# Optimization experiments

Measured on AMD Instinct MI355X. Metric: run time of the kernel, lower is better.

Reference implementation:

```python
import jax, jax.numpy as jnp
import numpy as np

N1, N2, N3, N4, D = 50000, 100000, 200000, 300000, 256


def setup_inputs() -> dict:
    key = jax.random.key(0)
    ks = jax.random.split(key, 10)
    feat = jax.random.normal(ks[0], (N1, D), dtype=jnp.float32) * 0.5  # scaled so level-4 products stay bounded
    c2a = jax.random.randint(ks[1], (N2,), 0, N1)
    c2b = jax.random.randint(ks[2], (N2,), 0, N1)
    c3a = jax.random.randint(ks[3], (N3,), 0, N2)
    c3b = jax.random.randint(ks[4], (N3,), 0, N2)
    c4a = jax.random.randint(ks[5], (N4,), 0, N3)
    c4b = jax.random.randint(ks[6], (N4,), 0, N3)
    W = jax.random.normal(ks[7], (D, D), dtype=jnp.float32) / jnp.sqrt(jnp.float32(D))
    b = jax.random.normal(ks[8], (D,), dtype=jnp.float32) * 0.01
    return {"feat": feat, "c2a": c2a, "c2b": c2b, "c3a": c3a, "c3b": c3b,
            "c4a": c4a, "c4b": c4b, "W": W, "b": b}


def _scatter_sum(h_parent, ca, cb, num_children):
    # each parent sends its feature to both children; children sum incoming messages
    z = jnp.zeros((num_children, h_parent.shape[1]), dtype=h_parent.dtype)
    return z.at[ca].add(h_parent).at[cb].add(h_parent)


def reference(feat, c2a, c2b, c3a, c3b, c4a, c4b, W, b):
    # upward: prod reduction over the two constituent subpaths (mailbox prod, dim=1)
    h1 = feat
    h2 = h1[c2a] * h1[c2b]            # [N2, D]
    h3 = h2[c3a] * h2[c3b]            # [N3, D]
    h4 = h3[c4a] * h3[c4b]            # [N4, D]
    # downward: sum-scatter parent -> children, h = h + h_down
    h3 = h3 + _scatter_sum(h4, c4a, c4b, h3.shape[0])
    h2 = h2 + _scatter_sum(h3, c3a, c3b, h2.shape[0])
    h1 = h1 + _scatter_sum(h2, c2a, c2b, h1.shape[0])
    # apply_nodes on n1: Linear + SiLU
    out = jax.nn.silu(h1 @ W + b)
    return out
```

## Files before the change

### kernel.cpp

```cpp
#include <hip/hip_runtime.h>
#include <cstdint>
#include <cstddef>

#define DD 256
#define DH 128
#define SCAN_BLK 256
#define SCAN_ELEMS 2048

__device__ __forceinline__ float4 f4mul(float4 a, float4 b) {
    return make_float4(a.x * b.x, a.y * b.y, a.z * b.z, a.w * b.w);
}
__device__ __forceinline__ float4 f4add(float4 a, float4 b) {
    return make_float4(a.x + b.x, a.y + b.y, a.z + b.z, a.w + b.w);
}
__device__ __forceinline__ float4 ldh4(const float* __restrict__ base, int row, int sl) {
    return ((const float4*)(base + (size_t)row * DH))[sl];
}
__device__ __forceinline__ float4 ldf4(const float* __restrict__ base, int row, int doff, int sl) {
    return ((const float4*)(base + (size_t)row * DD + doff))[sl];
}

__global__ void k_count_all(const int* __restrict__ c2a, const int* __restrict__ c2b,
                            const int* __restrict__ c3a, const int* __restrict__ c3b,
                            const int* __restrict__ c4a, const int* __restrict__ c4b,
                            int n2, int n3, int n4,
                            int* __restrict__ cnt4, int* __restrict__ cnt3,
                            int* __restrict__ cnt2) {
    int e = blockIdx.x * blockDim.x + threadIdx.x;
    if (e < n4) { atomicAdd(&cnt4[c4a[e]], 1); atomicAdd(&cnt4[c4b[e]], 1); }
    if (e < n3) { atomicAdd(&cnt3[c3a[e]], 1); atomicAdd(&cnt3[c3b[e]], 1); }
    if (e < n2) { atomicAdd(&cnt2[c2a[e]], 1); atomicAdd(&cnt2[c2b[e]], 1); }
}

__global__ void k_fill_all(const int* __restrict__ c2a, const int* __restrict__ c2b,
                           const int* __restrict__ c3a, const int* __restrict__ c3b,
                           const int* __restrict__ c4a, const int* __restrict__ c4b,
                           int n2, int n3, int n4,
                           int* __restrict__ cur4, int* __restrict__ cur3,
                           int* __restrict__ cur2,
                           int2* __restrict__ entp, int* __restrict__ ent3,
                           int* __restrict__ ent2) {
    int e = blockIdx.x * blockDim.x + threadIdx.x;
    if (e < n4) {
        int a = c4a[e], b = c4b[e];
        int2 prA = make_int2(c3a[b], c3b[b]);
        int2 prB = make_int2(c3a[a], c3b[a]);
        int pa = atomicAdd(&cur4[a], 1);
        int pb = atomicAdd(&cur4[b], 1);
        entp[pa] = prA;
        entp[pb] = prB;
    }
    if (e < n3) {
        int a = c3a[e], b = c3b[e];
        int pa = atomicAdd(&cur3[a], 1);
        int pb = atomicAdd(&cur3[b], 1);
        ent3[pa] = e;
        ent3[pb] = e;
    }
    if (e < n2) {
        int a = c2a[e], b = c2b[e];
        int pa = atomicAdd(&cur2[a], 1);
        int pb = atomicAdd(&cur2[b], 1);
        ent2[pa] = e;
        ent2[pb] = e;
    }
}

__global__ void k_block_sums(const int* __restrict__ cnt, int n, int* __restrict__ bsum) {
    __shared__ int sdata[SCAN_BLK];
    int base = blockIdx.x * SCAN_ELEMS;
    int s = 0;
#pragma unroll
    for (int k = 0; k < 8; ++k) {
        int idx = base + threadIdx.x + k * SCAN_BLK;
        if (idx < n) s += cnt[idx];
    }
    sdata[threadIdx.x] = s;
    __syncthreads();
    for (int off = SCAN_BLK / 2; off > 0; off >>= 1) {
        if (threadIdx.x < off) sdata[threadIdx.x] += sdata[threadIdx.x + off];
        __syncthreads();
    }
    if (threadIdx.x == 0) bsum[blockIdx.x] = sdata[0];
}

__global__ void k_scan_bsums(int* __restrict__ bsum, int nb, int* __restrict__ total_out) {
    if (threadIdx.x == 0 && blockIdx.x == 0) {
        int acc = 0;
        for (int b = 0; b < nb; ++b) { int v = bsum[b]; bsum[b] = acc; acc += v; }
        *total_out = acc;
    }
}

__global__ void k_scan_final(const int* __restrict__ cnt, int n,
                             const int* __restrict__ bsum, int* __restrict__ offs,
                             int* __restrict__ cursor) {
    __shared__ int sdata[SCAN_BLK];
    int base = blockIdx.x * SCAN_ELEMS;
    int t0 = base + threadIdx.x * 8;
    int loc[8];
    int s = 0;
#pragma unroll
    for (int k = 0; k < 8; ++k) {
        int idx = t0 + k;
        int v = (idx < n) ? cnt[idx] : 0;
        loc[k] = s;
        s += v;
    }
    sdata[threadIdx.x] = s;
    __syncthreads();
    int run = s;
    for (int off = 1; off < SCAN_BLK; off <<= 1) {
        int add = (threadIdx.x >= (unsigned)off) ? sdata[threadIdx.x - off] : 0;
        __syncthreads();
        run += add;
        sdata[threadIdx.x] = run;
        __syncthreads();
    }
    int texcl = run - s + bsum[blockIdx.x];
#pragma unroll
    for (int k = 0; k < 8; ++k) {
        int idx = t0 + k;
        if (idx < n) {
            int v = texcl + loc[k];
            offs[idx] = v;
            cursor[idx] = v;
        }
    }
}

__global__ void k_h2_half(const float* __restrict__ feat, const int* __restrict__ c2a,
                          const int* __restrict__ c2b, float* __restrict__ h2h,
                          int n2, int doff) {
    int q = blockIdx.x * 8 + (threadIdx.x >> 5);
    int sl = threadIdx.x & 31;
    if (q >= n2) return;
    float4 v = f4mul(ldf4(feat, c2a[q], doff, sl), ldf4(feat, c2b[q], doff, sl));
    ((float4*)(h2h + (size_t)q * DH))[sl] = v;
}

__global__ void k_h3tot_half(const float* __restrict__ h2h,
                             const int* __restrict__ c3a, const int* __restrict__ c3b,
                             const int* __restrict__ offs4, const int2* __restrict__ entp,
                             float* __restrict__ h3th, int lo, int hi) {
    int j = lo + blockIdx.x * 8 + (threadIdx.x >> 5);
    int sl = threadIdx.x & 31;
    if (j >= hi) return;
    float4 own = f4mul(ldh4(h2h, c3a[j], sl), ldh4(h2h, c3b[j], sl));
    float4 s = make_float4(0.f, 0.f, 0.f, 0.f);
    int e0 = offs4[j], e1 = offs4[j + 1];
    int e = e0;
    for (; e + 1 < e1; e += 2) {
        int2 p0 = entp[e], p1 = entp[e + 1];
        float4 a0 = ldh4(h2h, p0.x, sl), b0 = ldh4(h2h, p0.y, sl);
        float4 a1 = ldh4(h2h, p1.x, sl), b1 = ldh4(h2h, p1.y, sl);
        s = f4add(s, f4add(f4mul(a0, b0), f4mul(a1, b1)));
    }
    if (e < e1) {
        int2 p = entp[e];
        s = f4add(s, f4mul(ldh4(h2h, p.x, sl), ldh4(h2h, p.y, sl)));
    }
    float4 r = f4mul(own, make_float4(1.f + s.x, 1.f + s.y, 1.f + s.z, 1.f + s.w));
    ((float4*)(h3th + (size_t)(j - lo) * DH))[sl] = r;
}

__global__ void k_m2_half(const float* __restrict__ h2h,
                          const int* __restrict__ offs3, const int* __restrict__ ent3,
                          const float* __restrict__ h3th, float* __restrict__ dst,
                          int n2, int lo, int hi, int first) {
    int q = blockIdx.x * 8 + (threadIdx.x >> 5);
    int sl = threadIdx.x & 31;
    if (q >= n2) return;
    float4 h = first ? ldh4(h2h, q, sl) : ldh4(dst, q, sl);
    int f0 = offs3[q], f1 = offs3[q + 1];
    int f = f0;
    for (; f + 1 < f1; f += 2) {
        int j0 = ent3[f], j1 = ent3[f + 1];
        bool in0 = (j0 >= lo) && (j0 < hi);
        bool in1 = (j1 >= lo) && (j1 < hi);
        if (in0 && in1) {
            h = f4add(h, f4add(ldh4(h3th, j0 - lo, sl), ldh4(h3th, j1 - lo, sl)));
        } else if (in0) {
            h = f4add(h, ldh4(h3th, j0 - lo, sl));
        } else if (in1) {
            h = f4add(h, ldh4(h3th, j1 - lo, sl));
        }
    }
    if (f < f1) {
        int j0 = ent3[f];
        if (j0 >= lo && j0 < hi) h = f4add(h, ldh4(h3th, j0 - lo, sl));
    }
    ((float4*)(dst + (size_t)q * DH))[sl] = h;
}

__global__ void k_h1_half(const float* __restrict__ feat, const float* __restrict__ m2,
                          const int* __restrict__ offs2, const int* __restrict__ ent2,
                          float* __restrict__ out, int n1, int doff) {
    int i = blockIdx.x * 8 + (threadIdx.x >> 5);
    int sl = threadIdx.x & 31;
    if (i >= n1) return;
    float4 h = ldf4(feat, i, doff, sl);
    int e0 = offs2[i], e1 = offs2[i + 1];
    int e = e0;
    for (; e + 1 < e1; e += 2) {
        int q0 = ent2[e], q1 = ent2[e + 1];
        h = f4add(h, f4add(ldh4(m2, q0, sl), ldh4(m2, q1, sl)));
    }
    if (e < e1) h = f4add(h, ldh4(m2, ent2[e], sl));
    ((float4*)(out + (size_t)i * DD + doff))[sl] = h;
}

__device__ __forceinline__ float silu_f(float x) { return x / (1.0f + expf(-x)); }

__global__ __launch_bounds__(256) void k_gemm_silu(float* __restrict__ h,
                                                   const float* __restrict__ W,
                                                   const float* __restrict__ bias,
                                                   int n1) {
    __shared__ float As[32 * DD];
    const int t = threadIdx.x;
    const int row0 = blockIdx.x * 32;

    const float4* hv = (const float4*)h;
    float4* As4 = (float4*)As;
#pragma unroll
    for (int i = 0; i < 8; ++i) {
        int idx = t + i * 256;
        int r = idx >> 6, c = idx & 63;
        int gr = row0 + r;
        float4 v = make_float4(0.f, 0.f, 0.f, 0.f);
        if (gr < n1) v = hv[(size_t)gr * 64 + c];
        As4[idx] = v;
    }
    __syncthreads();

    const int rg = t >> 6;
    const int cg = t & 63;
    const float4* Wv = (const float4*)W;

    float4 acc[8];
#pragma unroll
    for (int r = 0; r < 8; ++r) acc[r] = make_float4(0.f, 0.f, 0.f, 0.f);

    for (int k = 0; k < DD; k += 4) {
        float4 a[8];
#pragma unroll
        for (int r = 0; r < 8; ++r)
            a[r] = *(const float4*)&As[(rg * 8 + r) * DD + k];
#pragma unroll
        for (int kk = 0; kk < 4; ++kk) {
            float4 w = Wv[(size_t)(k + kk) * 64 + cg];
#pragma unroll
            for (int r = 0; r < 8; ++r) {
                float av = (kk == 0) ? a[r].x : (kk == 1) ? a[r].y
                         : (kk == 2) ? a[r].z : a[r].w;
                acc[r].x += av * w.x;
                acc[r].y += av * w.y;
                acc[r].z += av * w.z;
                acc[r].w += av * w.w;
            }
        }
    }

    float4 bb = ((const float4*)bias)[cg];
    float4* ho = (float4*)h;
#pragma unroll
    for (int r = 0; r < 8; ++r) {
        int gr = row0 + rg * 8 + r;
        if (gr >= n1) continue;
        float4 x = acc[r];
        x.x = silu_f(x.x + bb.x);
        x.y = silu_f(x.y + bb.y);
        x.z = silu_f(x.z + bb.z);
        x.w = silu_f(x.w + bb.w);
        ho[(size_t)gr * 64 + cg] = x;
    }
}

static inline size_t al16(size_t x) { return (x + 15) & ~(size_t)15; }

extern "C" void kernel_launch(void* const* d_in, const int* in_sizes, int n_in,
                              void* d_out, int out_size, void* d_ws, size_t ws_size,
                              hipStream_t stream) {
    const float* feat = (const float*)d_in[0];
    const int* c2a = (const int*)d_in[1];
    const int* c2b = (const int*)d_in[2];
    const int* c3a = (const int*)d_in[3];
    const int* c3b = (const int*)d_in[4];
    const int* c4a = (const int*)d_in[5];
    const int* c4b = (const int*)d_in[6];
    const float* W = (const float*)d_in[7];
    const float* bias = (const float*)d_in[8];

    const int N1 = in_sizes[0] / DD;
    const int N2 = in_sizes[1];
    const int N3 = in_sizes[3];
    const int N4 = in_sizes[5];
    float* out = (float*)d_out;
    char* ws = (char*)d_ws;

    dim3 blk(256);
    auto rows_grid8 = [](int n) { return dim3((unsigned)((n + 7) / 8)); };
    auto thr_grid = [](int n) { return dim3((unsigned)((n + 255) / 256)); };

    size_t cnt4_b  = al16((size_t)N3 * 4);
    size_t cnt3_b  = al16((size_t)N2 * 4);
    size_t cnt2_b  = al16((size_t)N1 * 4);
    size_t cur4_b  = al16((size_t)N3 * 4);
    size_t cur3_b  = al16((size_t)N2 * 4);
    size_t cur2_b  = al16((size_t)N1 * 4);
    size_t bsum_b  = al16(4096);
    size_t offs4_b = al16((size_t)(N3 + 1) * 4);
    size_t entp_b  = al16((size_t)2 * N4 * 8);
    size_t offs3_b = al16((size_t)(N2 + 1) * 4);
    size_t ent3_b  = al16((size_t)2 * N3 * 4);
    size_t offs2_b = al16((size_t)(N1 + 1) * 4);
    size_t ent2_b  = al16((size_t)2 * N2 * 4);
    size_t fixed_b = cnt4_b + cnt3_b + cnt2_b + cur4_b + cur3_b + cur2_b + bsum_b +
                     offs4_b + entp_b + offs3_b + ent3_b + offs2_b + ent2_b;
    size_t h2h_b = (size_t)N2 * DH * sizeof(float);
    size_t h3th_full_b = (size_t)N3 * DH * sizeof(float);

    char* p = ws;
    int* cnt4  = (int*)p; p += cnt4_b;
    int* cnt3  = (int*)p; p += cnt3_b;
    int* cnt2  = (int*)p; p += cnt2_b;
    int* cur4  = (int*)p; p += cur4_b;
    int* cur3  = (int*)p; p += cur3_b;
    int* cur2  = (int*)p; p += cur2_b;
    int* bsum  = (int*)p; p += bsum_b;
    int* offs4 = (int*)p; p += offs4_b;
    int2* entp = (int2*)p; p += entp_b;
    int* offs3 = (int*)p; p += offs3_b;
    int* ent3  = (int*)p; p += ent3_b;
    int* offs2 = (int*)p; p += offs2_b;
    int* ent2  = (int*)p; p += ent2_b;
    float* h2h = (float*)p; p += h2h_b;

    bool single = (ws_size >= fixed_b + h2h_b + h3th_full_b);

    auto scan_offs = [&](int* cn, int nnode, int* offs, int* cursor) {
        int nb = (nnode + SCAN_ELEMS - 1) / SCAN_ELEMS;
        k_block_sums<<<dim3((unsigned)nb), dim3(SCAN_BLK), 0, stream>>>(cn, nnode, bsum);
        k_scan_bsums<<<dim3(1), dim3(64), 0, stream>>>(bsum, nb, offs + nnode);
        k_scan_final<<<dim3((unsigned)nb), dim3(SCAN_BLK), 0, stream>>>(cn, nnode, bsum,
                                                                        offs, cursor);
    };

    int maxE = N2 > N3 ? N2 : N3;
    if (N4 > maxE) maxE = N4;
    hipMemsetAsync(cnt4, 0, cnt4_b + cnt3_b + cnt2_b, stream);
    k_count_all<<<thr_grid(maxE), blk, 0, stream>>>(c2a, c2b, c3a, c3b, c4a, c4b,
                                                    N2, N3, N4, cnt4, cnt3, cnt2);
    scan_offs(cnt4, N3, offs4, cur4);
    scan_offs(cnt3, N2, offs3, cur3);
    scan_offs(cnt2, N1, offs2, cur2);
    k_fill_all<<<thr_grid(maxE), blk, 0, stream>>>(c2a, c2b, c3a, c3b, c4a, c4b,
                                                   N2, N3, N4, cur4, cur3, cur2,
                                                   entp, ent3, ent2);

    if (single) {
        float* h3th = (float*)p;
        for (int doff = 0; doff < DD; doff += DH) {
            k_h2_half<<<rows_grid8(N2), blk, 0, stream>>>(feat, c2a, c2b, h2h, N2, doff);
            k_h3tot_half<<<rows_grid8(N3), blk, 0, stream>>>(h2h, c3a, c3b, offs4, entp,
                                                             h3th, 0, N3);
            k_m2_half<<<rows_grid8(N2), blk, 0, stream>>>(h2h, offs3, ent3, h3th,
                                                          h2h, N2, 0, N3, 1);
            k_h1_half<<<rows_grid8(N1), blk, 0, stream>>>(feat, h2h, offs2, ent2,
                                                          out, N1, doff);
        }
    } else {
        float* m2h = (float*)p;
        char* pc = p + h2h_b;
        float* h3th = (float*)pc;
        size_t free_b = (ws_size > fixed_b + 2 * h2h_b) ? ws_size - fixed_b - 2 * h2h_b : 0;
        int chunk_rows = (int)(free_b / ((size_t)DH * sizeof(float)));
        if (chunk_rows > N3) chunk_rows = N3;
        if (chunk_rows < 1) chunk_rows = 1;
        int C = (N3 + chunk_rows - 1) / chunk_rows;
        chunk_rows = (N3 + C - 1) / C;

        for (int doff = 0; doff < DD; doff += DH) {
            k_h2_half<<<rows_grid8(N2), blk, 0, stream>>>(feat, c2a, c2b, h2h, N2, doff);
            int first = 1;
            for (int lo = 0; lo < N3; lo += chunk_rows) {
                int hi = lo + chunk_rows;
                if (hi > N3) hi = N3;
                k_h3tot_half<<<rows_grid8(hi - lo), blk, 0, stream>>>(h2h, c3a, c3b,
                                                                      offs4, entp,
                                                                      h3th, lo, hi);
                k_m2_half<<<rows_grid8(N2), blk, 0, stream>>>(h2h, offs3, ent3, h3th,
                                                              m2h, N2, lo, hi, first);
                first = 0;
            }
            k_h1_half<<<rows_grid8(N1), blk, 0, stream>>>(feat, m2h, offs2, ent2,
                                                          out, N1, doff);
        }
    }

    k_gemm_silu<<<dim3((unsigned)((N1 + 31) / 32)), blk, 0, stream>>>(out, W, bias, N1);
}
```

Baseline: 777.6 us.

## Scatter parent values into CSR slot order so children read contiguous rows

The producer kernels now write each h3 and m2 row straight into the child's CSR slot positions (pos3/pos2, recorded during fill). The downward-sum kernels then stream contiguous rows instead of gathering through index lists. Vector width also drops from float4 over 32 lanes to float2 over 64 lanes, so one wavefront covers one row. The cost is a duplicated slot buffer (2x rows) and more workspace, and tiered fallbacks are kept for when the workspace is too small.

```diff
diff --git a/kernel.cpp b/kernel.cpp
--- a/kernel.cpp
+++ b/kernel.cpp
@@ -7,17 +7,17 @@
 #define SCAN_BLK 256
 #define SCAN_ELEMS 2048
 
-__device__ __forceinline__ float4 f4mul(float4 a, float4 b) {
-    return make_float4(a.x * b.x, a.y * b.y, a.z * b.z, a.w * b.w);
-}
-__device__ __forceinline__ float4 f4add(float4 a, float4 b) {
-    return make_float4(a.x + b.x, a.y + b.y, a.z + b.z, a.w + b.w);
-}
-__device__ __forceinline__ float4 ldh4(const float* __restrict__ base, int row, int sl) {
-    return ((const float4*)(base + (size_t)row * DH))[sl];
-}
-__device__ __forceinline__ float4 ldf4(const float* __restrict__ base, int row, int doff, int sl) {
-    return ((const float4*)(base + (size_t)row * DD + doff))[sl];
+__device__ __forceinline__ float2 mul2(float2 a, float2 b) {
+    return make_float2(a.x * b.x, a.y * b.y);
+}
+__device__ __forceinline__ float2 add2(float2 a, float2 b) {
+    return make_float2(a.x + b.x, a.y + b.y);
+}
+__device__ __forceinline__ float2 ldh(const float* __restrict__ base, int row, int lane) {
+    return ((const float2*)(base + (size_t)row * DH))[lane];
+}
+__device__ __forceinline__ float2 ldf(const float* __restrict__ base, int row, int doff, int lane) {
+    return ((const float2*)(base + (size_t)row * DD + doff))[lane];
 }
 
 __global__ void k_count_all(const int* __restrict__ c2a, const int* __restrict__ c2b,
@@ -39,7 +39,8 @@
                            int* __restrict__ cur4, int* __restrict__ cur3,
                            int* __restrict__ cur2,
                            int2* __restrict__ entp, int* __restrict__ ent3,
-                           int* __restrict__ ent2) {
+                           int* __restrict__ ent2,
+                           int* __restrict__ pos3, int* __restrict__ pos2) {
     int e = blockIdx.x * blockDim.x + threadIdx.x;
     if (e < n4) {
         int a = c4a[e], b = c4b[e];
@@ -56,6 +57,8 @@
         int pb = atomicAdd(&cur3[b], 1);
         ent3[pa] = e;
         ent3[pb] = e;
+        pos3[2 * e] = pa;
+        pos3[2 * e + 1] = pb;
     }
     if (e < n2) {
         int a = c2a[e], b = c2b[e];
@@ -63,6 +66,8 @@
         int pb = atomicAdd(&cur2[b], 1);
         ent2[pa] = e;
         ent2[pb] = e;
+        pos2[2 * e] = pa;
+        pos2[2 * e + 1] = pb;
     }
 }
 
@@ -132,46 +137,110 @@
 __global__ void k_h2_half(const float* __restrict__ feat, const int* __restrict__ c2a,
                           const int* __restrict__ c2b, float* __restrict__ h2h,
                           int n2, int doff) {
-    int q = blockIdx.x * 8 + (threadIdx.x >> 5);
-    int sl = threadIdx.x & 31;
+    int q = blockIdx.x * 4 + (threadIdx.x >> 6);
+    int lane = threadIdx.x & 63;
     if (q >= n2) return;
-    float4 v = f4mul(ldf4(feat, c2a[q], doff, sl), ldf4(feat, c2b[q], doff, sl));
-    ((float4*)(h2h + (size_t)q * DH))[sl] = v;
+    float2 v = mul2(ldf(feat, c2a[q], doff, lane), ldf(feat, c2b[q], doff, lane));
+    ((float2*)(h2h + (size_t)q * DH))[lane] = v;
+}
+
+__global__ void k_h3tot_slot(const float* __restrict__ h2h,
+                             const int* __restrict__ c3a, const int* __restrict__ c3b,
+                             const int* __restrict__ offs4, const int2* __restrict__ entp,
+                             const int* __restrict__ pos3, float* __restrict__ S3,
+                             int n3) {
+    int j = blockIdx.x * 4 + (threadIdx.x >> 6);
+    int lane = threadIdx.x & 63;
+    if (j >= n3) return;
+    float2 own = mul2(ldh(h2h, c3a[j], lane), ldh(h2h, c3b[j], lane));
+    float2 s = make_float2(0.f, 0.f);
+    int e0 = offs4[j], e1 = offs4[j + 1];
+    int e = e0;
+    for (; e + 1 < e1; e += 2) {
+        int2 p0 = entp[e], p1 = entp[e + 1];
+        float2 a0 = ldh(h2h, p0.x, lane), b0 = ldh(h2h, p0.y, lane);
+        float2 a1 = ldh(h2h, p1.x, lane), b1 = ldh(h2h, p1.y, lane);
+        s = add2(s, add2(mul2(a0, b0), mul2(a1, b1)));
+    }
+    if (e < e1) {
+        int2 p = entp[e];
+        s = add2(s, mul2(ldh(h2h, p.x, lane), ldh(h2h, p.y, lane)));
+    }
+    float2 r = mul2(own, make_float2(1.f + s.x, 1.f + s.y));
+    int s0 = pos3[2 * j], s1 = pos3[2 * j + 1];
+    ((float2*)(S3 + (size_t)s0 * DH))[lane] = r;
+    ((float2*)(S3 + (size_t)s1 * DH))[lane] = r;
 }
 
 __global__ void k_h3tot_half(const float* __restrict__ h2h,
                              const int* __restrict__ c3a, const int* __restrict__ c3b,
                              const int* __restrict__ offs4, const int2* __restrict__ entp,
                              float* __restrict__ h3th, int lo, int hi) {
-    int j = lo + blockIdx.x * 8 + (threadIdx.x >> 5);
-    int sl = threadIdx.x & 31;
+    int j = lo + blockIdx.x * 4 + (threadIdx.x >> 6);
+    int lane = threadIdx.x & 63;
     if (j >= hi) return;
-    float4 own = f4mul(ldh4(h2h, c3a[j], sl), ldh4(h2h, c3b[j], sl));
-    float4 s = make_float4(0.f, 0.f, 0.f, 0.f);
+    float2 own = mul2(ldh(h2h, c3a[j], lane), ldh(h2h, c3b[j], lane));
+    float2 s = make_float2(0.f, 0.f);
     int e0 = offs4[j], e1 = offs4[j + 1];
     int e = e0;
     for (; e + 1 < e1; e += 2) {
         int2 p0 = entp[e], p1 = entp[e + 1];
-        float4 a0 = ldh4(h2h, p0.x, sl), b0 = ldh4(h2h, p0.y, sl);
-        float4 a1 = ldh4(h2h, p1.x, sl), b1 = ldh4(h2h, p1.y, sl);
-        s = f4add(s, f4add(f4mul(a0, b0), f4mul(a1, b1)));
+        float2 a0 = ldh(h2h, p0.x, lane), b0 = ldh(h2h, p0.y, lane);
+        float2 a1 = ldh(h2h, p1.x, lane), b1 = ldh(h2h, p1.y, lane);
+        s = add2(s, add2(mul2(a0, b0), mul2(a1, b1)));
     }
     if (e < e1) {
         int2 p = entp[e];
-        s = f4add(s, f4mul(ldh4(h2h, p.x, sl), ldh4(h2h, p.y, sl)));
-    }
-    float4 r = f4mul(own, make_float4(1.f + s.x, 1.f + s.y, 1.f + s.z, 1.f + s.w));
-    ((float4*)(h3th + (size_t)(j - lo) * DH))[sl] = r;
+        s = add2(s, mul2(ldh(h2h, p.x, lane), ldh(h2h, p.y, lane)));
+    }
+    float2 r = mul2(own, make_float2(1.f + s.x, 1.f + s.y));
+    ((float2*)(h3th + (size_t)(j - lo) * DH))[lane] = r;
+}
+
+__global__ void k_m2_stream_inplace(float* __restrict__ h2h,
+                                    const int* __restrict__ offs3,
+                                    const float* __restrict__ S3, int n2) {
+    int q = blockIdx.x * 4 + (threadIdx.x >> 6);
+    int lane = threadIdx.x & 63;
+    if (q >= n2) return;
+    float2 h = ldh(h2h, q, lane);
+    int f0 = offs3[q], f1 = offs3[q + 1];
+    int f = f0;
+    for (; f + 1 < f1; f += 2) {
+        h = add2(h, add2(ldh(S3, f, lane), ldh(S3, f + 1, lane)));
+    }
+    if (f < f1) h = add2(h, ldh(S3, f, lane));
+    ((float2*)(h2h + (size_t)q * DH))[lane] = h;
+}
+
+__global__ void k_m2_stream_slots(const float* __restrict__ h2h,
+                                  const int* __restrict__ offs3,
+                                  const float* __restrict__ S3,
+                                  const int* __restrict__ pos2,
+                                  float* __restrict__ S2, int n2) {
+    int q = blockIdx.x * 4 + (threadIdx.x >> 6);
+    int lane = threadIdx.x & 63;
+    if (q >= n2) return;
+    float2 h = ldh(h2h, q, lane);
+    int f0 = offs3[q], f1 = offs3[q + 1];
+    int f = f0;
+    for (; f + 1 < f1; f += 2) {
+        h = add2(h, add2(ldh(S3, f, lane), ldh(S3, f + 1, lane)));
+    }
+    if (f < f1) h = add2(h, ldh(S3, f, lane));
+    int s0 = pos2[2 * q], s1 = pos2[2 * q + 1];
+    ((float2*)(S2 + (size_t)s0 * DH))[lane] = h;
+    ((float2*)(S2 + (size_t)s1 * DH))[lane] = h;
 }
 
 __global__ void k_m2_half(const float* __restrict__ h2h,
                           const int* __restrict__ offs3, const int* __restrict__ ent3,
                           const float* __restrict__ h3th, float* __restrict__ dst,
                           int n2, int lo, int hi, int first) {
-    int q = blockIdx.x * 8 + (threadIdx.x >> 5);
-    int sl = threadIdx.x & 31;
+    int q = blockIdx.x * 4 + (threadIdx.x >> 6);
+    int lane = threadIdx.x & 63;
     if (q >= n2) return;
-    float4 h = first ? ldh4(h2h, q, sl) : ldh4(dst, q, sl);
+    float2 h = first ? ldh(h2h, q, lane) : ldh(dst, q, lane);
     int f0 = offs3[q], f1 = offs3[q + 1];
     int f = f0;
     for (; f + 1 < f1; f += 2) {
@@ -179,35 +248,52 @@
         bool in0 = (j0 >= lo) && (j0 < hi);
         bool in1 = (j1 >= lo) && (j1 < hi);
         if (in0 && in1) {
-            h = f4add(h, f4add(ldh4(h3th, j0 - lo, sl), ldh4(h3th, j1 - lo, sl)));
+            h = add2(h, add2(ldh(h3th, j0 - lo, lane), ldh(h3th, j1 - lo, lane)));
         } else if (in0) {
-            h = f4add(h, ldh4(h3th, j0 - lo, sl));
+            h = add2(h, ldh(h3th, j0 - lo, lane));
         } else if (in1) {
-            h = f4add(h, ldh4(h3th, j1 - lo, sl));
+            h = add2(h, ldh(h3th, j1 - lo, lane));
         }
     }
     if (f < f1) {
         int j0 = ent3[f];
-        if (j0 >= lo && j0 < hi) h = f4add(h, ldh4(h3th, j0 - lo, sl));
-    }
-    ((float4*)(dst + (size_t)q * DH))[sl] = h;
+        if (j0 >= lo && j0 < hi) h = add2(h, ldh(h3th, j0 - lo, lane));
+    }
+    ((float2*)(dst + (size_t)q * DH))[lane] = h;
+}
+
+__global__ void k_h1_stream(const float* __restrict__ feat,
+                            const int* __restrict__ offs2,
+                            const float* __restrict__ S2,
+                            float* __restrict__ out, int n1, int doff) {
+    int i = blockIdx.x * 4 + (threadIdx.x >> 6);
+    int lane = threadIdx.x & 63;
+    if (i >= n1) return;
+    float2 h = ldf(feat, i, doff, lane);
+    int e0 = offs2[i], e1 = offs2[i + 1];
+    int e = e0;
+    for (; e + 1 < e1; e += 2) {
+        h = add2(h, add2(ldh(S2, e, lane), ldh(S2, e + 1, lane)));
+    }
+    if (e < e1) h = add2(h, ldh(S2, e, lane));
+    ((float2*)(out + (size_t)i * DD + doff))[lane] = h;
 }
 
 __global__ void k_h1_half(const float* __restrict__ feat, const float* __restrict__ m2,
                           const int* __restrict__ offs2, const int* __restrict__ ent2,
                           float* __restrict__ out, int n1, int doff) {
-    int i = blockIdx.x * 8 + (threadIdx.x >> 5);
-    int sl = threadIdx.x & 31;
+    int i = blockIdx.x * 4 + (threadIdx.x >> 6);
+    int lane = threadIdx.x & 63;
     if (i >= n1) return;
-    float4 h = ldf4(feat, i, doff, sl);
+    float2 h = ldf(feat, i, doff, lane);
     int e0 = offs2[i], e1 = offs2[i + 1];
     int e = e0;
     for (; e + 1 < e1; e += 2) {
         int q0 = ent2[e], q1 = ent2[e + 1];
-        h = f4add(h, f4add(ldh4(m2, q0, sl), ldh4(m2, q1, sl)));
-    }
-    if (e < e1) h = f4add(h, ldh4(m2, ent2[e], sl));
-    ((float4*)(out + (size_t)i * DD + doff))[sl] = h;
+        h = add2(h, add2(ldh(m2, q0, lane), ldh(m2, q1, lane)));
+    }
+    if (e < e1) h = add2(h, ldh(m2, ent2[e], lane));
+    ((float2*)(out + (size_t)i * DD + doff))[lane] = h;
 }
 
 __device__ __forceinline__ float silu_f(float x) { return x / (1.0f + expf(-x)); }
@@ -299,7 +385,7 @@
     char* ws = (char*)d_ws;
 
     dim3 blk(256);
-    auto rows_grid8 = [](int n) { return dim3((unsigned)((n + 7) / 8)); };
+    auto rows_grid4 = [](int n) { return dim3((unsigned)((n + 3) / 4)); };
     auto thr_grid = [](int n) { return dim3((unsigned)((n + 255) / 256)); };
 
     size_t cnt4_b  = al16((size_t)N3 * 4);
@@ -315,10 +401,15 @@
     size_t ent3_b  = al16((size_t)2 * N3 * 4);
     size_t offs2_b = al16((size_t)(N1 + 1) * 4);
     size_t ent2_b  = al16((size_t)2 * N2 * 4);
+    size_t pos3_b  = al16((size_t)2 * N3 * 4);
+    size_t pos2_b  = al16((size_t)2 * N2 * 4);
     size_t fixed_b = cnt4_b + cnt3_b + cnt2_b + cur4_b + cur3_b + cur2_b + bsum_b +
-                     offs4_b + entp_b + offs3_b + ent3_b + offs2_b + ent2_b;
+                     offs4_b + entp_b + offs3_b + ent3_b + offs2_b + ent2_b +
+                     pos3_b + pos2_b;
     size_t h2h_b = (size_t)N2 * DH * sizeof(float);
-    size_t h3th_full_b = (size_t)N3 * DH * sizeof(float);
+    size_t h3th_b = (size_t)N3 * DH * sizeof(float);
+    size_t S3_b  = (size_t)2 * N3 * DH * sizeof(float);
+    size_t S2_b  = (size_t)2 * N2 * DH * sizeof(float);
 
     char* p = ws;
     int* cnt4  = (int*)p; p += cnt4_b;
@@ -334,9 +425,14 @@
     int* ent3  = (int*)p; p += ent3_b;
     int* offs2 = (int*)p; p += offs2_b;
     int* ent2  = (int*)p; p += ent2_b;
+    int* pos3  = (int*)p; p += pos3_b;
+    int* pos2  = (int*)p; p += pos2_b;
     float* h2h = (float*)p; p += h2h_b;
-
-    bool single = (ws_size >= fixed_b + h2h_b + h3th_full_b);
+    char* dyn = p;
+
+    const bool tierAp = (ws_size >= fixed_b + h2h_b + S3_b + S2_b);
+    const bool tierA  = !tierAp && (ws_size >= fixed_b + h2h_b + S3_b);
+    const bool tierB  = !tierAp && !tierA && (ws_size >= fixed_b + h2h_b + h3th_b);
 
     auto scan_offs = [&](int* cn, int nnode, int* offs, int* cursor) {
         int nb = (nnode + SCAN_ELEMS - 1) / SCAN_ELEMS;
@@ -356,23 +452,43 @@
     scan_offs(cnt2, N1, offs2, cur2);
     k_fill_all<<<thr_grid(maxE), blk, 0, stream>>>(c2a, c2b, c3a, c3b, c4a, c4b,
                                                    N2, N3, N4, cur4, cur3, cur2,
-                                                   entp, ent3, ent2);
-
-    if (single) {
-        float* h3th = (float*)p;
+                                                   entp, ent3, ent2, pos3, pos2);
+
+    if (tierAp) {
+        float* S3 = (float*)dyn;
+        float* S2 = (float*)(dyn + S3_b);
         for (int doff = 0; doff < DD; doff += DH) {
-            k_h2_half<<<rows_grid8(N2), blk, 0, stream>>>(feat, c2a, c2b, h2h, N2, doff);
-            k_h3tot_half<<<rows_grid8(N3), blk, 0, stream>>>(h2h, c3a, c3b, offs4, entp,
+            k_h2_half<<<rows_grid4(N2), blk, 0, stream>>>(feat, c2a, c2b, h2h, N2, doff);
+            k_h3tot_slot<<<rows_grid4(N3), blk, 0, stream>>>(h2h, c3a, c3b, offs4, entp,
+                                                             pos3, S3, N3);
+            k_m2_stream_slots<<<rows_grid4(N2), blk, 0, stream>>>(h2h, offs3, S3,
+                                                                  pos2, S2, N2);
+            k_h1_stream<<<rows_grid4(N1), blk, 0, stream>>>(feat, offs2, S2, out, N1, doff);
+        }
+    } else if (tierA) {
+        float* S3 = (float*)dyn;
+        for (int doff = 0; doff < DD; doff += DH) {
+            k_h2_half<<<rows_grid4(N2), blk, 0, stream>>>(feat, c2a, c2b, h2h, N2, doff);
+            k_h3tot_slot<<<rows_grid4(N3), blk, 0, stream>>>(h2h, c3a, c3b, offs4, entp,
+                                                             pos3, S3, N3);
+            k_m2_stream_inplace<<<rows_grid4(N2), blk, 0, stream>>>(h2h, offs3, S3, N2);
+            k_h1_half<<<rows_grid4(N1), blk, 0, stream>>>(feat, h2h, offs2, ent2,
+                                                          out, N1, doff);
+        }
+    } else if (tierB) {
+        float* h3th = (float*)dyn;
+        for (int doff = 0; doff < DD; doff += DH) {
+            k_h2_half<<<rows_grid4(N2), blk, 0, stream>>>(feat, c2a, c2b, h2h, N2, doff);
+            k_h3tot_half<<<rows_grid4(N3), blk, 0, stream>>>(h2h, c3a, c3b, offs4, entp,
                                                              h3th, 0, N3);
-            k_m2_half<<<rows_grid8(N2), blk, 0, stream>>>(h2h, offs3, ent3, h3th,
+            k_m2_half<<<rows_grid4(N2), blk, 0, stream>>>(h2h, offs3, ent3, h3th,
                                                           h2h, N2, 0, N3, 1);
-            k_h1_half<<<rows_grid8(N1), blk, 0, stream>>>(feat, h2h, offs2, ent2,
+            k_h1_half<<<rows_grid4(N1), blk, 0, stream>>>(feat, h2h, offs2, ent2,
                                                           out, N1, doff);
         }
     } else {
-        float* m2h = (float*)p;
-        char* pc = p + h2h_b;
-        float* h3th = (float*)pc;
+        float* m2h = (float*)dyn;
+        float* h3th = (float*)(dyn + h2h_b);
         size_t free_b = (ws_size > fixed_b + 2 * h2h_b) ? ws_size - fixed_b - 2 * h2h_b : 0;
         int chunk_rows = (int)(free_b / ((size_t)DH * sizeof(float)));
         if (chunk_rows > N3) chunk_rows = N3;
@@ -381,19 +497,19 @@
         chunk_rows = (N3 + C - 1) / C;
 
         for (int doff = 0; doff < DD; doff += DH) {
-            k_h2_half<<<rows_grid8(N2), blk, 0, stream>>>(feat, c2a, c2b, h2h, N2, doff);
+            k_h2_half<<<rows_grid4(N2), blk, 0, stream>>>(feat, c2a, c2b, h2h, N2, doff);
             int first = 1;
             for (int lo = 0; lo < N3; lo += chunk_rows) {
                 int hi = lo + chunk_rows;
                 if (hi > N3) hi = N3;
-                k_h3tot_half<<<rows_grid8(hi - lo), blk, 0, stream>>>(h2h, c3a, c3b,
+                k_h3tot_half<<<rows_grid4(hi - lo), blk, 0, stream>>>(h2h, c3a, c3b,
                                                                       offs4, entp,
                                                                       h3th, lo, hi);
-                k_m2_half<<<rows_grid8(N2), blk, 0, stream>>>(h2h, offs3, ent3, h3th,
+                k_m2_half<<<rows_grid4(N2), blk, 0, stream>>>(h2h, offs3, ent3, h3th,
                                                               m2h, N2, lo, hi, first);
                 first = 0;
             }
-            k_h1_half<<<rows_grid8(N1), blk, 0, stream>>>(feat, m2h, offs2, ent2,
+            k_h1_half<<<rows_grid4(N1), blk, 0, stream>>>(feat, m2h, offs2, ent2,
                                                           out, N1, doff);
         }
     }
```

Result: no change. 778.0 us (+0.1%).

## Split feature dim into quarters, materialize h3, and scatter level-3 results to CSR slots

Applied to the files above, without the earlier changes.

The feature dimension is now processed in four 64-wide slices instead of two 128-wide halves, with one float per lane in place of float4. A separate h3 buffer is materialized per slice, so the level-4 gather reads one h3 row per neighbor instead of two h2 rows plus a multiply. Level-3 totals are written directly into CSR-ordered slots through a new pos3 map, which lets the m2 pass stream contiguously rather than gather. This trades fewer random gathers and a smaller working set for twice as many kernel launches and narrower loads, and the chunked fallback path appears incorrect (its offsets do not line up).

```diff
diff --git a/kernel.cpp b/kernel.cpp
--- a/kernel.cpp
+++ b/kernel.cpp
@@ -3,22 +3,9 @@
 #include <cstddef>
 
 #define DD 256
-#define DH 128
+#define DQ 64
 #define SCAN_BLK 256
 #define SCAN_ELEMS 2048
-
-__device__ __forceinline__ float4 f4mul(float4 a, float4 b) {
-    return make_float4(a.x * b.x, a.y * b.y, a.z * b.z, a.w * b.w);
-}
-__device__ __forceinline__ float4 f4add(float4 a, float4 b) {
-    return make_float4(a.x + b.x, a.y + b.y, a.z + b.z, a.w + b.w);
-}
-__device__ __forceinline__ float4 ldh4(const float* __restrict__ base, int row, int sl) {
-    return ((const float4*)(base + (size_t)row * DH))[sl];
-}
-__device__ __forceinline__ float4 ldf4(const float* __restrict__ base, int row, int doff, int sl) {
-    return ((const float4*)(base + (size_t)row * DD + doff))[sl];
-}
 
 __global__ void k_count_all(const int* __restrict__ c2a, const int* __restrict__ c2b,
                             const int* __restrict__ c3a, const int* __restrict__ c3b,
@@ -38,17 +25,15 @@
                            int n2, int n3, int n4,
                            int* __restrict__ cur4, int* __restrict__ cur3,
                            int* __restrict__ cur2,
-                           int2* __restrict__ entp, int* __restrict__ ent3,
-                           int* __restrict__ ent2) {
+                           int* __restrict__ ent4o, int* __restrict__ ent3,
+                           int* __restrict__ ent2, int* __restrict__ pos3) {
     int e = blockIdx.x * blockDim.x + threadIdx.x;
     if (e < n4) {
         int a = c4a[e], b = c4b[e];
-        int2 prA = make_int2(c3a[b], c3b[b]);
-        int2 prB = make_int2(c3a[a], c3b[a]);
         int pa = atomicAdd(&cur4[a], 1);
         int pb = atomicAdd(&cur4[b], 1);
-        entp[pa] = prA;
-        entp[pb] = prB;
+        ent4o[pa] = b;
+        ent4o[pb] = a;
     }
     if (e < n3) {
         int a = c3a[e], b = c3b[e];
@@ -56,6 +41,8 @@
         int pb = atomicAdd(&cur3[b], 1);
         ent3[pa] = e;
         ent3[pb] = e;
+        pos3[2 * e] = pa;
+        pos3[2 * e + 1] = pb;
     }
     if (e < n2) {
         int a = c2a[e], b = c2b[e];
@@ -129,85 +116,107 @@
     }
 }
 
-__global__ void k_h2_half(const float* __restrict__ feat, const int* __restrict__ c2a,
-                          const int* __restrict__ c2b, float* __restrict__ h2h,
-                          int n2, int doff) {
-    int q = blockIdx.x * 8 + (threadIdx.x >> 5);
-    int sl = threadIdx.x & 31;
+__global__ void k_h2_q(const float* __restrict__ feat, const int* __restrict__ c2a,
+                       const int* __restrict__ c2b, float* __restrict__ h2q,
+                       int n2, int doff) {
+    int q = blockIdx.x * 4 + (threadIdx.x >> 6);
+    int lane = threadIdx.x & 63;
     if (q >= n2) return;
-    float4 v = f4mul(ldf4(feat, c2a[q], doff, sl), ldf4(feat, c2b[q], doff, sl));
-    ((float4*)(h2h + (size_t)q * DH))[sl] = v;
-}
-
-__global__ void k_h3tot_half(const float* __restrict__ h2h,
-                             const int* __restrict__ c3a, const int* __restrict__ c3b,
-                             const int* __restrict__ offs4, const int2* __restrict__ entp,
-                             float* __restrict__ h3th, int lo, int hi) {
-    int j = lo + blockIdx.x * 8 + (threadIdx.x >> 5);
-    int sl = threadIdx.x & 31;
-    if (j >= hi) return;
-    float4 own = f4mul(ldh4(h2h, c3a[j], sl), ldh4(h2h, c3b[j], sl));
-    float4 s = make_float4(0.f, 0.f, 0.f, 0.f);
+    float a = feat[(size_t)c2a[q] * DD + doff + lane];
+    float b = feat[(size_t)c2b[q] * DD + doff + lane];
+    h2q[(size_t)q * DQ + lane] = a * b;
+}
+
+__global__ void k_h3_q(const float* __restrict__ h2q, const int* __restrict__ c3a,
+                       const int* __restrict__ c3b, float* __restrict__ h3q, int n3) {
+    int j = blockIdx.x * 4 + (threadIdx.x >> 6);
+    int lane = threadIdx.x & 63;
+    if (j >= n3) return;
+    float a = h2q[(size_t)c3a[j] * DQ + lane];
+    float b = h2q[(size_t)c3b[j] * DQ + lane];
+    h3q[(size_t)j * DQ + lane] = a * b;
+}
+
+__global__ void k_h3tot_slot_q(const float* __restrict__ h3q,
+                               const int* __restrict__ offs4,
+                               const int* __restrict__ ent4o,
+                               const int* __restrict__ pos3,
+                               float* __restrict__ S3, int n3) {
+    int j = blockIdx.x * 4 + (threadIdx.x >> 6);
+    int lane = threadIdx.x & 63;
+    if (j >= n3) return;
+    float own = h3q[(size_t)j * DQ + lane];
+    float s = 0.f;
     int e0 = offs4[j], e1 = offs4[j + 1];
     int e = e0;
-    for (; e + 1 < e1; e += 2) {
-        int2 p0 = entp[e], p1 = entp[e + 1];
-        float4 a0 = ldh4(h2h, p0.x, sl), b0 = ldh4(h2h, p0.y, sl);
-        float4 a1 = ldh4(h2h, p1.x, sl), b1 = ldh4(h2h, p1.y, sl);
-        s = f4add(s, f4add(f4mul(a0, b0), f4mul(a1, b1)));
-    }
-    if (e < e1) {
-        int2 p = entp[e];
-        s = f4add(s, f4mul(ldh4(h2h, p.x, sl), ldh4(h2h, p.y, sl)));
-    }
-    float4 r = f4mul(own, make_float4(1.f + s.x, 1.f + s.y, 1.f + s.z, 1.f + s.w));
-    ((float4*)(h3th + (size_t)(j - lo) * DH))[sl] = r;
-}
-
-__global__ void k_m2_half(const float* __restrict__ h2h,
-                          const int* __restrict__ offs3, const int* __restrict__ ent3,
-                          const float* __restrict__ h3th, float* __restrict__ dst,
-                          int n2, int lo, int hi, int first) {
-    int q = blockIdx.x * 8 + (threadIdx.x >> 5);
-    int sl = threadIdx.x & 31;
+    for (; e + 3 < e1; e += 4) {
+        float v0 = h3q[(size_t)ent4o[e] * DQ + lane];
+        float v1 = h3q[(size_t)ent4o[e + 1] * DQ + lane];
+        float v2 = h3q[(size_t)ent4o[e + 2] * DQ + lane];
+        float v3 = h3q[(size_t)ent4o[e + 3] * DQ + lane];
+        s += (v0 + v1) + (v2 + v3);
+    }
+    for (; e < e1; ++e) s += h3q[(size_t)ent4o[e] * DQ + lane];
+    float r = own * (1.f + s);
+    S3[(size_t)pos3[2 * j] * DQ + lane] = r;
+    S3[(size_t)pos3[2 * j + 1] * DQ + lane] = r;
+}
+
+__global__ void k_h3tot_q(const float* __restrict__ h3q,
+                          const int* __restrict__ offs4,
+                          const int* __restrict__ ent4o,
+                          float* __restrict__ h3t, int n3) {
+    int j = blockIdx.x * 4 + (threadIdx.x >> 6);
+    int lane = threadIdx.x & 63;
+    if (j >= n3) return;
+    float own = h3q[(size_t)j * DQ + lane];
+    float s = 0.f;
+    int e0 = offs4[j], e1 = offs4[j + 1];
+    for (int e = e0; e < e1; ++e) s += h3q[(size_t)ent4o[e] * DQ + lane];
+    h3t[(size_t)j * DQ + lane] = own * (1.f + s);
+}
+
+__global__ void k_m2_stream_q(float* __restrict__ h2q, const int* __restrict__ offs3,
+                              const float* __restrict__ S3, int n2) {
+    int q = blockIdx.x * 4 + (threadIdx.x >> 6);
+    int lane = threadIdx.x & 63;
     if (q >= n2) return;
-    float4 h = first ? ldh4(h2h, q, sl) : ldh4(dst, q, sl);
+    float h = h2q[(size_t)q * DQ + lane];
     int f0 = offs3[q], f1 = offs3[q + 1];
     int f = f0;
     for (; f + 1 < f1; f += 2) {
-        int j0 = ent3[f], j1 = ent3[f + 1];
-        bool in0 = (j0 >= lo) && (j0 < hi);
-        bool in1 = (j1 >= lo) && (j1 < hi);
-        if (in0 && in1) {
-            h = f4add(h, f4add(ldh4(h3th, j0 - lo, sl), ldh4(h3th, j1 - lo, sl)));
-        } else if (in0) {
-            h = f4add(h, ldh4(h3th, j0 - lo, sl));
-        } else if (in1) {
-            h = f4add(h, ldh4(h3th, j1 - lo, sl));
-        }
-    }
-    if (f < f1) {
-        int j0 = ent3[f];
-        if (j0 >= lo && j0 < hi) h = f4add(h, ldh4(h3th, j0 - lo, sl));
-    }
-    ((float4*)(dst + (size_t)q * DH))[sl] = h;
-}
-
-__global__ void k_h1_half(const float* __restrict__ feat, const float* __restrict__ m2,
-                          const int* __restrict__ offs2, const int* __restrict__ ent2,
-                          float* __restrict__ out, int n1, int doff) {
-    int i = blockIdx.x * 8 + (threadIdx.x >> 5);
-    int sl = threadIdx.x & 31;
+        h += S3[(size_t)f * DQ + lane] + S3[(size_t)(f + 1) * DQ + lane];
+    }
+    if (f < f1) h += S3[(size_t)f * DQ + lane];
+    h2q[(size_t)q * DQ + lane] = h;
+}
+
+__global__ void k_m2_gather_q(float* __restrict__ h2q, const int* __restrict__ offs3,
+                              const int* __restrict__ ent3,
+                              const float* __restrict__ h3t, int n2) {
+    int q = blockIdx.x * 4 + (threadIdx.x >> 6);
+    int lane = threadIdx.x & 63;
+    if (q >= n2) return;
+    float h = h2q[(size_t)q * DQ + lane];
+    int f0 = offs3[q], f1 = offs3[q + 1];
+    for (int f = f0; f < f1; ++f) h += h3t[(size_t)ent3[f] * DQ + lane];
+    h2q[(size_t)q * DQ + lane] = h;
+}
+
+__global__ void k_h1_q(const float* __restrict__ feat, const float* __restrict__ m2,
+                       const int* __restrict__ offs2, const int* __restrict__ ent2,
+                       float* __restrict__ out, int n1, int doff) {
+    int i = blockIdx.x * 4 + (threadIdx.x >> 6);
+    int lane = threadIdx.x & 63;
     if (i >= n1) return;
-    float4 h = ldf4(feat, i, doff, sl);
+    float h = feat[(size_t)i * DD + doff + lane];
     int e0 = offs2[i], e1 = offs2[i + 1];
     int e = e0;
     for (; e + 1 < e1; e += 2) {
-        int q0 = ent2[e], q1 = ent2[e + 1];
-        h = f4add(h, f4add(ldh4(m2, q0, sl), ldh4(m2, q1, sl)));
-    }
-    if (e < e1) h = f4add(h, ldh4(m2, ent2[e], sl));
-    ((float4*)(out + (size_t)i * DD + doff))[sl] = h;
+        h += m2[(size_t)ent2[e] * DQ + lane] + m2[(size_t)ent2[e + 1] * DQ + lane];
+    }
+    if (e < e1) h += m2[(size_t)ent2[e] * DQ + lane];
+    out[(size_t)i * DD + doff + lane] = h;
 }
 
 __device__ __forceinline__ float silu_f(float x) { return x / (1.0f + expf(-x)); }
@@ -299,7 +308,7 @@
     char* ws = (char*)d_ws;
 
     dim3 blk(256);
-    auto rows_grid8 = [](int n) { return dim3((unsigned)((n + 7) / 8)); };
+    auto rows_grid4 = [](int n) { return dim3((unsigned)((n + 3) / 4)); };
     auto thr_grid = [](int n) { return dim3((unsigned)((n + 255) / 256)); };
 
     size_t cnt4_b  = al16((size_t)N3 * 4);
@@ -310,15 +319,17 @@
     size_t cur2_b  = al16((size_t)N1 * 4);
     size_t bsum_b  = al16(4096);
     size_t offs4_b = al16((size_t)(N3 + 1) * 4);
-    size_t entp_b  = al16((size_t)2 * N4 * 8);
+    size_t ent4o_b = al16((size_t)2 * N4 * 4);
     size_t offs3_b = al16((size_t)(N2 + 1) * 4);
     size_t ent3_b  = al16((size_t)2 * N3 * 4);
     size_t offs2_b = al16((size_t)(N1 + 1) * 4);
     size_t ent2_b  = al16((size_t)2 * N2 * 4);
+    size_t pos3_b  = al16((size_t)2 * N3 * 4);
     size_t fixed_b = cnt4_b + cnt3_b + cnt2_b + cur4_b + cur3_b + cur2_b + bsum_b +
-                     offs4_b + entp_b + offs3_b + ent3_b + offs2_b + ent2_b;
-    size_t h2h_b = (size_t)N2 * DH * sizeof(float);
-    size_t h3th_full_b = (size_t)N3 * DH * sizeof(float);
+                     offs4_b + ent4o_b + offs3_b + ent3_b + offs2_b + ent2_b + pos3_b;
+    size_t h2q_b = (size_t)N2 * DQ * sizeof(float);
+    size_t h3q_b = (size_t)N3 * DQ * sizeof(float);
+    size_t S3q_b = (size_t)2 * N3 * DQ * sizeof(float);
 
     char* p = ws;
     int* cnt4  = (int*)p; p += cnt4_b;
@@ -329,14 +340,18 @@
     int* cur2  = (int*)p; p += cur2_b;
     int* bsum  = (int*)p; p += bsum_b;
     int* offs4 = (int*)p; p += offs4_b;
-    int2* entp = (int2*)p; p += entp_b;
+    int* ent4o = (int*)p; p += ent4o_b;
     int* offs3 = (int*)p; p += offs3_b;
     int* ent3  = (int*)p; p += ent3_b;
     int* offs2 = (int*)p; p += offs2_b;
     int* ent2  = (int*)p; p += ent2_b;
-    float* h2h = (float*)p; p += h2h_b;
-
-    bool single = (ws_size >= fixed_b + h2h_b + h3th_full_b);
+    int* pos3  = (int*)p; p += pos3_b;
+    float* h2q = (float*)p; p += h2q_b;
+    float* h3q = (float*)p; p += h3q_b;
+    char* dyn = p;
+
+    const bool tierA = (ws_size >= fixed_b + h2q_b + h3q_b + S3q_b);
+    const bool tierB = !tierA && (ws_size >= fixed_b + h2q_b + h3q_b + h3q_b);
 
     auto scan_offs = [&](int* cn, int nnode, int* offs, int* cursor) {
         int nb = (nnode + SCAN_ELEMS - 1) / SCAN_ELEMS;
@@ -356,45 +371,52 @@
     scan_offs(cnt2, N1, offs2, cur2);
     k_fill_all<<<thr_grid(maxE), blk, 0, stream>>>(c2a, c2b, c3a, c3b, c4a, c4b,
                                                    N2, N3, N4, cur4, cur3, cur2,
-                                                   entp, ent3, ent2);
-
-    if (single) {
-        float* h3th = (float*)p;
-        for (int doff = 0; doff < DD; doff += DH) {
-            k_h2_half<<<rows_grid8(N2), blk, 0, stream>>>(feat, c2a, c2b, h2h, N2, doff);
-            k_h3tot_half<<<rows_grid8(N3), blk, 0, stream>>>(h2h, c3a, c3b, offs4, entp,
-                                                             h3th, 0, N3);
-            k_m2_half<<<rows_grid8(N2), blk, 0, stream>>>(h2h, offs3, ent3, h3th,
-                                                          h2h, N2, 0, N3, 1);
-            k_h1_half<<<rows_grid8(N1), blk, 0, stream>>>(feat, h2h, offs2, ent2,
-                                                          out, N1, doff);
+                                                   ent4o, ent3, ent2, pos3);
+
+    if (tierA) {
+        float* S3 = (float*)dyn;
+        for (int doff = 0; doff < DD; doff += DQ) {
+            k_h2_q<<<rows_grid4(N2), blk, 0, stream>>>(feat, c2a, c2b, h2q, N2, doff);
+            k_h3_q<<<rows_grid4(N3), blk, 0, stream>>>(h2q, c3a, c3b, h3q, N3);
+            k_h3tot_slot_q<<<rows_grid4(N3), blk, 0, stream>>>(h3q, offs4, ent4o,
+                                                               pos3, S3, N3);
+            k_m2_stream_q<<<rows_grid4(N2), blk, 0, stream>>>(h2q, offs3, S3, N2);
+            k_h1_q<<<rows_grid4(N1), blk, 0, stream>>>(feat, h2q, offs2, ent2,
+                                                       out, N1, doff);
+        }
+    } else if (tierB) {
+        float* h3t = (float*)dyn;
+        for (int doff = 0; doff < DD; doff += DQ) {
+            k_h2_q<<<rows_grid4(N2), blk, 0, stream>>>(feat, c2a, c2b, h2q, N2, doff);
+            k_h3_q<<<rows_grid4(N3), blk, 0, stream>>>(h2q, c3a, c3b, h3q, N3);
+            k_h3tot_q<<<rows_grid4(N3), blk, 0, stream>>>(h3q, offs4, ent4o, h3t, N3);
+            k_m2_gather_q<<<rows_grid4(N2), blk, 0, stream>>>(h2q, offs3, ent3, h3t, N2);
+            k_h1_q<<<rows_grid4(N1), blk, 0, stream>>>(feat, h2q, offs2, ent2,
+                                                       out, N1, doff);
         }
     } else {
-        float* m2h = (float*)p;
-        char* pc = p + h2h_b;
-        float* h3th = (float*)pc;
-        size_t free_b = (ws_size > fixed_b + 2 * h2h_b) ? ws_size - fixed_b - 2 * h2h_b : 0;
-        int chunk_rows = (int)(free_b / ((size_t)DH * sizeof(float)));
+        float* h3t_chunk = (float*)dyn;
+        size_t free_b = (ws_size > fixed_b + h2q_b + h3q_b)
+                      ? ws_size - fixed_b - h2q_b - h3q_b : 0;
+        int chunk_rows = (int)(free_b / ((size_t)DQ * sizeof(float)));
         if (chunk_rows > N3) chunk_rows = N3;
         if (chunk_rows < 1) chunk_rows = 1;
         int C = (N3 + chunk_rows - 1) / chunk_rows;
         chunk_rows = (N3 + C - 1) / C;
-
-        for (int doff = 0; doff < DD; doff += DH) {
-            k_h2_half<<<rows_grid8(N2), blk, 0, stream>>>(feat, c2a, c2b, h2h, N2, doff);
-            int first = 1;
+        for (int doff = 0; doff < DD; doff += DQ) {
+            k_h2_q<<<rows_grid4(N2), blk, 0, stream>>>(feat, c2a, c2b, h2q, N2, doff);
+            k_h3_q<<<rows_grid4(N3), blk, 0, stream>>>(h2q, c3a, c3b, h3q, N3);
             for (int lo = 0; lo < N3; lo += chunk_rows) {
                 int hi = lo + chunk_rows;
                 if (hi > N3) hi = N3;
-                k_h3tot_half<<<rows_grid8(hi - lo), blk, 0, stream>>>(h2h, c3a, c3b,
-                                                                      offs4, entp,
-                                                                      h3th, lo, hi);
-                k_m2_half<<<rows_grid8(N2), blk, 0, stream>>>(h2h, offs3, ent3, h3th,
-                                                              m2h, N2, lo, hi, first);
-                first = 0;
+                k_h3tot_q<<<rows_grid4(hi - lo), blk, 0, stream>>>(h3q + (size_t)lo * DQ - (size_t)lo * DQ,
+                                                                   offs4 + lo, ent4o,
+                                                                   h3t_chunk - 0, hi - lo);
             }
-            k_h1_half<<<rows_grid8(N1), blk, 0, stream>>>(feat, m2h, offs2, ent2,
-                                                          out, N1, doff);
+            k_m2_gather_q<<<rows_grid4(N2), blk, 0, stream>>>(h2q, offs3, ent3,
+                                                              h3t_chunk, N2);
+            k_h1_q<<<rows_grid4(N1), blk, 0, stream>>>(feat, h2q, offs2, ent2,
+                                                       out, N1, doff);
         }
     }
 
```

Result: slower. 995.0 us (+28.0%).
